# Kernel tuning notes

Measured on AMD Instinct MI355X. Metric: run time of the kernel, lower is better.

## Reference

```python
import jax, jax.numpy as jnp
import numpy as np

QMIN, QMAX = -128, 127  # 8-bit symmetric
EPS = 1e-8

def _fake_quant(v, scale, axis):
    # per-channel symmetric fake quant: round, clamp, dequant
    shape = [1] * v.ndim
    shape[axis] = -1
    s = (jnp.abs(scale) + EPS).reshape(shape)
    q = jnp.clip(jnp.round(v / s), QMIN, QMAX)
    return q * s

def setup_inputs() -> dict:
    key = jax.random.key(0)
    k1, k2, k3, k4, k5 = jax.random.split(key, 5)
    B, C_in, L = 32, 512, 4096
    C_out, K = 512, 3
    return {
        "x": jax.random.normal(k1, (B, C_in, L), dtype=jnp.float32),
        "weight": jax.random.normal(k2, (C_out, C_in, K), dtype=jnp.float32) * 0.05,
        "bias": jax.random.normal(k3, (C_out,), dtype=jnp.float32) * 0.1,
        "a_scale": jax.random.uniform(k4, (C_in,), dtype=jnp.float32, minval=0.01, maxval=0.1),
        "w_scale": jax.random.uniform(k5, (C_out,), dtype=jnp.float32, minval=0.001, maxval=0.01),
    }

def reference(x, weight, bias, a_scale, w_scale):
    # activations: per-channel (axis=1 of NCL) symmetric int8 fake-quant
    x_hat = _fake_quant(x, a_scale, axis=1)
    # weights: per-out-channel (axis=0 of OIK) symmetric int8 fake-quant
    w_hat = _fake_quant(weight, w_scale, axis=0)
    out = jax.lax.conv_general_dilated(
        x_hat, w_hat,
        window_strides=(1,), padding=[(1, 1)], rhs_dilation=(1,),
        dimension_numbers=("NCH", "OIH", "NCH"))
    return out + bias[None, :, None]
```

## Files before the change

### kernel.cpp

```cpp
#include <hip/hip_runtime.h>
#include <hip/hip_bf16.h>
#include <stdint.h>

#define BATCH 32
#define CIN   512
#define LLEN  4096
#define COUT  512
#define KW    3
#define KTOT  (CIN * KW)
#define LPAD  (LLEN + 2)
#define EPSQ  1e-8f

#define BM 256
#define BN 256
#define BK 32
#define NT (KTOT / BK)
#define TILE_ELEMS (BM * BK)

typedef __bf16 bf16x8 __attribute__((ext_vector_type(8)));
typedef float  floatx4 __attribute__((ext_vector_type(4)));

__device__ __forceinline__ void async_load16(const void* gptr, void* ldsptr) {
    __builtin_amdgcn_global_load_lds(
        (const __attribute__((address_space(1))) void*)gptr,
        (__attribute__((address_space(3))) void*)ldsptr,
        16, 0, 0);
}

__global__ void zero_pad_kernel(uint32_t* __restrict__ qxT_u32) {
    int idx = blockIdx.x * blockDim.x + threadIdx.x;
    int b = idx >> 9;
    int r = (idx >> 8) & 1;
    int c = idx & 255;
    size_t row = (size_t)b * LPAD + (r ? (LPAD - 1) : 0);
    qxT_u32[row * (CIN / 2) + c] = 0u;
}

__global__ __launch_bounds__(256) void quantx_kernel(
        const float* __restrict__ x,
        const float* __restrict__ a_scale,
        __bf16* __restrict__ qxT) {
    __shared__ __bf16 qs[64][66];
    const int i0 = blockIdx.x * 64;
    const int l0 = blockIdx.y * 64;
    const int b  = blockIdx.z;
    const int tid = threadIdx.x;

    const int f4   = tid & 15;
    const int irow = tid >> 4;
    #pragma unroll
    for (int p = 0; p < 4; ++p) {
        int i = p * 16 + irow;
        float s = fabsf(a_scale[i0 + i]) + EPSQ;
        float inv = 1.0f / s;
        const floatx4* xrow = (const floatx4*)(x + ((size_t)(b * CIN + i0 + i)) * LLEN + l0);
        floatx4 v = xrow[f4];
        #pragma unroll
        for (int j = 0; j < 4; ++j) {
            float q = fminf(fmaxf(rintf(v[j] * inv), -128.0f), 127.0f);
            qs[f4 * 4 + j][i] = (__bf16)q;
        }
    }
    __syncthreads();

    const int c4 = tid & 15;
    const int rr = tid >> 4;
    uint2* outp = (uint2*)(qxT + ((size_t)b * LPAD + (l0 + 1)) * CIN + i0);
    #pragma unroll
    for (int p = 0; p < 4; ++p) {
        int l = p * 16 + rr;
        const uint32_t* qrow = (const uint32_t*)&qs[l][0];
        uint2 u;
        u.x = qrow[2 * c4];
        u.y = qrow[2 * c4 + 1];
        outp[(size_t)l * (CIN / 4) + c4] = u;
    }
}

__global__ void wfold_kernel(
        const float* __restrict__ w,
        const float* __restrict__ a_scale,
        const float* __restrict__ w_scale,
        __bf16* __restrict__ Wf) {
    int idx = blockIdx.x * blockDim.x + threadIdx.x;
    if (idx >= COUT * KTOT) return;
    int o   = idx / KTOT;
    int rem = idx - o * KTOT;
    int k = rem >> 9;
    int i = rem & 511;
    float sw = fabsf(w_scale[o]) + EPSQ;
    float sa = fabsf(a_scale[i]) + EPSQ;
    float q = fminf(fmaxf(rintf(w[((size_t)o * CIN + i) * KW + k] / sw), -128.0f), 127.0f);
    Wf[idx] = (__bf16)(q * sa * sw);
}

__global__ __launch_bounds__(512, 2) void qconv_gemm(
        const __bf16* __restrict__ Wf,
        const __bf16* __restrict__ qxT,
        const float* __restrict__ bias,
        float* __restrict__ out) {
    __shared__ __attribute__((aligned(16))) __bf16 As[4][TILE_ELEMS];
    __shared__ __attribute__((aligned(16))) __bf16 Bs[4][TILE_ELEMS];

    const int tid = threadIdx.x;

    int flat = blockIdx.x + gridDim.x * (blockIdx.y + gridDim.y * blockIdx.z);
    int logical = (flat & 7) * 128 + (flat >> 3);
    const int m0 = (logical & 1) * BM;
    const int l0 = ((logical >> 1) & 15) * BN;
    const int b  = logical >> 5;

    const int wave  = tid >> 6;
    const int lane  = tid & 63;
    const int wm    = wave >> 2;
    const int wn    = wave & 3;
    const int row16 = lane & 15;
    const int quad  = lane >> 4;

    const __bf16* qxb = qxT + (size_t)b * LPAD * CIN;

    floatx4 acc[8][4];
    #pragma unroll
    for (int mt = 0; mt < 8; ++mt)
        #pragma unroll
        for (int nt = 0; nt < 4; ++nt)
            acc[mt][nt] = (floatx4){0.f, 0.f, 0.f, 0.f};

    const int ca0 = tid,        ca1 = 512 + tid;
    const int ra0 = ca0 >> 2,   ra1 = ca1 >> 2;
    const int ga0 = (ca0 & 3) ^ (ra0 & 3);
    const int ga1 = (ca1 & 3) ^ (ra1 & 3);
    const __bf16* aptr0 = Wf  + (size_t)(m0 + ra0) * KTOT + ga0 * 8;
    const __bf16* aptr1 = Wf  + (size_t)(m0 + ra1) * KTOT + ga1 * 8;
    const __bf16* bptr0 = qxb + (size_t)(l0 + ra0) * CIN  + ga0 * 8;
    const __bf16* bptr1 = qxb + (size_t)(l0 + ra1) * CIN  + ga1 * 8;

    auto STAGE = [&](int t) {
        const int kk0  = t * BK;
        const int kblk = kk0 >> 9;
        const int i0   = kk0 & 511;
        const int slot = t & 3;
        char* abase = (char*)&As[slot][0];
        char* bbase = (char*)&Bs[slot][0];
        async_load16(aptr0 + kk0,                        abase + ca0 * 16);
        async_load16(aptr1 + kk0,                        abase + ca1 * 16);
        async_load16(bptr0 + (size_t)kblk * CIN + i0,    bbase + ca0 * 16);
        async_load16(bptr1 + (size_t)kblk * CIN + i0,    bbase + ca1 * 16);
    };

    STAGE(0); STAGE(1); STAGE(2);

    for (int t = 0; t < NT; ++t) {
        __builtin_amdgcn_sched_barrier(0);
        __builtin_amdgcn_s_barrier();
        __builtin_amdgcn_sched_barrier(0);

        if (t + 3 < NT) STAGE(t + 3);

        if (t < NT - 3)      asm volatile("s_waitcnt vmcnt(12)" ::: "memory");
        else if (t == NT-3)  asm volatile("s_waitcnt vmcnt(8)"  ::: "memory");
        else if (t == NT-2)  asm volatile("s_waitcnt vmcnt(4)"  ::: "memory");
        else                 asm volatile("s_waitcnt vmcnt(0)"  ::: "memory");

        __builtin_amdgcn_sched_barrier(0);
        __builtin_amdgcn_s_barrier();
        __builtin_amdgcn_sched_barrier(0);

        const int slot = t & 3;
        const __bf16* Ab = &As[slot][0];
        const __bf16* Bb = &Bs[slot][0];

        bf16x8 af[8], bfr[4];
        #pragma unroll
        for (int mt = 0; mt < 8; ++mt) {
            int arow = wm * 128 + mt * 16 + row16;
            int js   = quad ^ (arow & 3);
            af[mt] = *(const bf16x8*)(Ab + arow * BK + js * 8);
        }
        #pragma unroll
        for (int nt = 0; nt < 4; ++nt) {
            int brow = wn * 64 + nt * 16 + row16;
            int js   = quad ^ (brow & 3);
            bfr[nt] = *(const bf16x8*)(Bb + brow * BK + js * 8);
        }

        __builtin_amdgcn_s_setprio(1);
        #pragma unroll
        for (int mt = 0; mt < 8; ++mt)
            #pragma unroll
            for (int nt = 0; nt < 4; ++nt)
                acc[mt][nt] = __builtin_amdgcn_mfma_f32_16x16x32_bf16(
                    af[mt], bfr[nt], acc[mt][nt], 0, 0, 0);
        __builtin_amdgcn_s_setprio(0);
    }

    float* outb = out + ((size_t)b * COUT + m0) * LLEN;
    #pragma unroll
    for (int mt = 0; mt < 8; ++mt) {
        #pragma unroll
        for (int r = 0; r < 4; ++r) {
            int o = wm * 128 + mt * 16 + quad * 4 + r;
            float bv = bias[m0 + o];
            #pragma unroll
            for (int nt = 0; nt < 4; ++nt) {
                int l = l0 + wn * 64 + nt * 16 + row16;
                outb[(size_t)o * LLEN + l] = acc[mt][nt][r] + bv;
            }
        }
    }
}

extern "C" void kernel_launch(void* const* d_in, const int* in_sizes, int n_in,
                              void* d_out, int out_size, void* d_ws, size_t ws_size,
                              hipStream_t stream) {
    const float* x       = (const float*)d_in[0];
    const float* weight  = (const float*)d_in[1];
    const float* bias    = (const float*)d_in[2];
    const float* a_scale = (const float*)d_in[3];
    const float* w_scale = (const float*)d_in[4];
    float* out = (float*)d_out;

    __bf16* Wf  = (__bf16*)d_ws;
    __bf16* qxT = (__bf16*)((char*)d_ws + (size_t)COUT * KTOT * sizeof(__bf16));

    wfold_kernel<<<dim3((COUT * KTOT) / 256), dim3(256), 0, stream>>>(
        weight, a_scale, w_scale, Wf);
    zero_pad_kernel<<<dim3(64), dim3(256), 0, stream>>>((uint32_t*)qxT);
    quantx_kernel<<<dim3(CIN / 64, LLEN / 64, BATCH), dim3(256), 0, stream>>>(
        x, a_scale, qxT);
    qconv_gemm<<<dim3(COUT / BM, LLEN / BN, BATCH), dim3(512), 0, stream>>>(
        Wf, qxT, bias, out);
}
```

Baseline: 712.0 us.

## Restructure GEMM mainloop into 8-phase ping-pong schedule with BK=64

```diff
diff --git a/kernel.cpp b/kernel.cpp
--- a/kernel.cpp
+++ b/kernel.cpp
@@ -13,9 +13,10 @@
 
 #define BM 256
 #define BN 256
-#define BK 32
-#define NT (KTOT / BK)
-#define TILE_ELEMS (BM * BK)
+#define BK 64
+#define NTILES (KTOT / BK)
+#define NI (NTILES / 2)
+#define SLOT_ELEMS (BM * BK)
 
 typedef __bf16 bf16x8 __attribute__((ext_vector_type(8)));
 typedef float  floatx4 __attribute__((ext_vector_type(4)));
@@ -94,13 +95,55 @@
     Wf[idx] = (__bf16)(q * sa * sw);
 }
 
+
+#define BARR() do { __builtin_amdgcn_sched_barrier(0); \
+                    __builtin_amdgcn_s_barrier();      \
+                    __builtin_amdgcn_sched_barrier(0); } while (0)
+#define LGKM0() do { asm volatile("s_waitcnt lgkmcnt(0)" ::: "memory"); \
+                     __builtin_amdgcn_sched_barrier(0); } while (0)
+#define VMW(n) do { asm volatile("s_waitcnt vmcnt(" #n ")" ::: "memory"); \
+                    __builtin_amdgcn_sched_barrier(0); } while (0)
+
+#define STG_A(tau, q) async_load16(Wf  + aoff[q] + (tau) * 64, \
+        (char*)&As[(tau) & 1][0] + doff[q])
+#define STG_B(tau, q) async_load16(qxb + boff[q] + (tau) * 64, \
+        (char*)&Bs[(tau) & 1][0] + doff[q])
+
+#define RD_AF(Ab, qm) do { \
+    _Pragma("unroll") for (int mti = 0; mti < 4; ++mti) { \
+        _Pragma("unroll") for (int ks = 0; ks < 2; ++ks) { \
+            int arow = wm * 128 + ((qm) * 4 + mti) * 16 + row16; \
+            int js   = (ks * 4 + quad) ^ (arow & 7); \
+            af[mti][ks] = *(const bf16x8*)((Ab) + arow * 64 + js * 8); \
+        } } } while (0)
+
+#define RD_BF(Bb, dst, qn) do { \
+    _Pragma("unroll") for (int nti = 0; nti < 2; ++nti) { \
+        _Pragma("unroll") for (int ks = 0; ks < 2; ++ks) { \
+            int brow = wn * 64 + ((qn) * 2 + nti) * 16 + row16; \
+            int js   = (ks * 4 + quad) ^ (brow & 7); \
+            dst[nti][ks] = *(const bf16x8*)((Bb) + brow * 64 + js * 8); \
+        } } } while (0)
+
+#define MFMAQ(qm, qn, bsrc) do { \
+    __builtin_amdgcn_s_setprio(1); \
+    _Pragma("unroll") for (int mti = 0; mti < 4; ++mti) { \
+        _Pragma("unroll") for (int nti = 0; nti < 2; ++nti) { \
+            _Pragma("unroll") for (int ks = 0; ks < 2; ++ks) { \
+                acc[(qm) * 4 + mti][(qn) * 2 + nti] = \
+                    __builtin_amdgcn_mfma_f32_16x16x32_bf16( \
+                        af[mti][ks], bsrc[nti][ks], \
+                        acc[(qm) * 4 + mti][(qn) * 2 + nti], 0, 0, 0); \
+            } } } \
+    __builtin_amdgcn_s_setprio(0); } while (0)
+
 __global__ __launch_bounds__(512, 2) void qconv_gemm(
         const __bf16* __restrict__ Wf,
         const __bf16* __restrict__ qxT,
         const float* __restrict__ bias,
         float* __restrict__ out) {
-    __shared__ __attribute__((aligned(16))) __bf16 As[4][TILE_ELEMS];
-    __shared__ __attribute__((aligned(16))) __bf16 Bs[4][TILE_ELEMS];
+    __shared__ __attribute__((aligned(16))) __bf16 As[2][SLOT_ELEMS];
+    __shared__ __attribute__((aligned(16))) __bf16 Bs[2][SLOT_ELEMS];
 
     const int tid = threadIdx.x;
 
@@ -126,72 +169,80 @@
         for (int nt = 0; nt < 4; ++nt)
             acc[mt][nt] = (floatx4){0.f, 0.f, 0.f, 0.f};
 
-    const int ca0 = tid,        ca1 = 512 + tid;
-    const int ra0 = ca0 >> 2,   ra1 = ca1 >> 2;
-    const int ga0 = (ca0 & 3) ^ (ra0 & 3);
-    const int ga1 = (ca1 & 3) ^ (ra1 & 3);
-    const __bf16* aptr0 = Wf  + (size_t)(m0 + ra0) * KTOT + ga0 * 8;
-    const __bf16* aptr1 = Wf  + (size_t)(m0 + ra1) * KTOT + ga1 * 8;
-    const __bf16* bptr0 = qxb + (size_t)(l0 + ra0) * CIN  + ga0 * 8;
-    const __bf16* bptr1 = qxb + (size_t)(l0 + ra1) * CIN  + ga1 * 8;
-
-    auto STAGE = [&](int t) {
-        const int kk0  = t * BK;
-        const int kblk = kk0 >> 9;
-        const int i0   = kk0 & 511;
-        const int slot = t & 3;
-        char* abase = (char*)&As[slot][0];
-        char* bbase = (char*)&Bs[slot][0];
-        async_load16(aptr0 + kk0,                        abase + ca0 * 16);
-        async_load16(aptr1 + kk0,                        abase + ca1 * 16);
-        async_load16(bptr0 + (size_t)kblk * CIN + i0,    bbase + ca0 * 16);
-        async_load16(bptr1 + (size_t)kblk * CIN + i0,    bbase + ca1 * 16);
-    };
-
-    STAGE(0); STAGE(1); STAGE(2);
-
-    for (int t = 0; t < NT; ++t) {
-        __builtin_amdgcn_sched_barrier(0);
-        __builtin_amdgcn_s_barrier();
-        __builtin_amdgcn_sched_barrier(0);
-
-        if (t + 3 < NT) STAGE(t + 3);
-
-        if (t < NT - 3)      asm volatile("s_waitcnt vmcnt(12)" ::: "memory");
-        else if (t == NT-3)  asm volatile("s_waitcnt vmcnt(8)"  ::: "memory");
-        else if (t == NT-2)  asm volatile("s_waitcnt vmcnt(4)"  ::: "memory");
-        else                 asm volatile("s_waitcnt vmcnt(0)"  ::: "memory");
-
-        __builtin_amdgcn_sched_barrier(0);
-        __builtin_amdgcn_s_barrier();
-        __builtin_amdgcn_sched_barrier(0);
-
-        const int slot = t & 3;
-        const __bf16* Ab = &As[slot][0];
-        const __bf16* Bb = &Bs[slot][0];
-
-        bf16x8 af[8], bfr[4];
-        #pragma unroll
-        for (int mt = 0; mt < 8; ++mt) {
-            int arow = wm * 128 + mt * 16 + row16;
-            int js   = quad ^ (arow & 3);
-            af[mt] = *(const bf16x8*)(Ab + arow * BK + js * 8);
-        }
-        #pragma unroll
-        for (int nt = 0; nt < 4; ++nt) {
-            int brow = wn * 64 + nt * 16 + row16;
-            int js   = quad ^ (brow & 3);
-            bfr[nt] = *(const bf16x8*)(Bb + brow * BK + js * 8);
-        }
-
-        __builtin_amdgcn_s_setprio(1);
-        #pragma unroll
-        for (int mt = 0; mt < 8; ++mt)
-            #pragma unroll
-            for (int nt = 0; nt < 4; ++nt)
-                acc[mt][nt] = __builtin_amdgcn_mfma_f32_16x16x32_bf16(
-                    af[mt], bfr[nt], acc[mt][nt], 0, 0, 0);
-        __builtin_amdgcn_s_setprio(0);
+    int aoff[4], boff[4], doff[4];
+    #pragma unroll
+    for (int q = 0; q < 4; ++q) {
+        int c = q * 512 + tid;
+        int r = c >> 3;
+        int g = (c & 7) ^ (r & 7);
+        aoff[q] = (m0 + r) * KTOT + g * 8;
+        boff[q] = (l0 + r) * CIN  + g * 8;
+        doff[q] = c * 16;
+    }
+
+    bf16x8 af[4][2], bf0[2][2], bf1[2][2];
+
+    STG_A(0, 0); STG_A(0, 1); STG_A(0, 2); STG_A(0, 3);
+    STG_B(0, 0); STG_B(0, 1); STG_B(0, 2); STG_B(0, 3);
+    STG_A(1, 0); STG_A(1, 1);
+    VMW(2);
+    BARR();
+
+    for (int i = 0; i < NI; ++i) {
+        const int t1 = 2 * i + 1, t2 = 2 * i + 2, t3 = 2 * i + 3;
+        const __bf16* Ab0 = &As[0][0];
+        const __bf16* Bb0 = &Bs[0][0];
+        const __bf16* Ab1 = &As[1][0];
+        const __bf16* Bb1 = &Bs[1][0];
+        const bool more = (i + 1 < NI);
+
+        RD_BF(Bb0, bf0, 0); RD_AF(Ab0, 0);
+        STG_A(t1, 2); STG_A(t1, 3);
+        BARR(); LGKM0();
+        MFMAQ(0, 0, bf0);
+        BARR();
+
+        RD_BF(Bb0, bf1, 1);
+        STG_B(t1, 0); STG_B(t1, 1);
+        BARR(); LGKM0();
+        MFMAQ(0, 1, bf1);
+        BARR();
+
+        RD_AF(Ab0, 1);
+        STG_B(t1, 2); STG_B(t1, 3);
+        BARR(); LGKM0();
+        MFMAQ(1, 1, bf1);
+        BARR();
+
+        if (more) { STG_A(t2, 0); STG_A(t2, 1); }
+        BARR(); LGKM0();
+        MFMAQ(1, 0, bf0);
+        if (more) { VMW(2); } else { VMW(0); }
+        BARR();
+
+        RD_BF(Bb1, bf0, 0); RD_AF(Ab1, 0);
+        if (more) { STG_A(t2, 2); STG_A(t2, 3); }
+        BARR(); LGKM0();
+        MFMAQ(0, 0, bf0);
+        BARR();
+
+        RD_BF(Bb1, bf1, 1);
+        if (more) { STG_B(t2, 0); STG_B(t2, 1); }
+        BARR(); LGKM0();
+        MFMAQ(0, 1, bf1);
+        BARR();
+
+        RD_AF(Ab1, 1);
+        if (more) { STG_B(t2, 2); STG_B(t2, 3); }
+        BARR(); LGKM0();
+        MFMAQ(1, 1, bf1);
+        BARR();
+
+        if (more) { STG_A(t3, 0); STG_A(t3, 1); }
+        BARR(); LGKM0();
+        MFMAQ(1, 0, bf0);
+        VMW(2);
+        BARR();
     }
 
     float* outb = out + ((size_t)b * COUT + m0) * LLEN;
```

New measurement: 644.3 us. -9.5%, faster.
